# Kernel tuning notes

Measured on AMD Instinct MI355X. Metric: run time of the kernel, lower is better.

The kernel has to match this reference:

```python
import jax, jax.numpy as jnp
import numpy as np

PRIOR = 0.2
TEMP = 1.0
THRESHOLD = 0.5
B, L, D, H = 8, 4096, 768, 512


def setup_inputs() -> dict:
    key = jax.random.key(0)
    k1, k2, k3, k4 = jax.random.split(key, 4)
    hidden = jax.random.normal(k1, (B, L, D), jnp.float32)
    # MLP params: Linear(D,H) -> ReLU -> Linear(H,1)
    W1 = jax.random.normal(k2, (D, H), jnp.float32) / np.sqrt(D).astype(np.float32)
    b1 = jnp.zeros((H,), jnp.float32)
    W2 = jax.random.normal(k3, (H, 1), jnp.float32) / np.sqrt(H).astype(np.float32)
    b2 = jnp.zeros((1,), jnp.float32)
    # pre-sampled uniform noise for the RelaxedBernoulli logistic reparameterization
    noise_u = jax.random.uniform(k4, (B, L), jnp.float32, minval=1e-6, maxval=1.0 - 1e-6)
    return dict(hidden=hidden, W1=W1, b1=b1, W2=W2, b2=b2, noise_u=noise_u)


def reference(hidden, W1, b1, W2, b2, noise_u):
    bs, seq_len, model_dim = hidden.shape
    # boundary MLP -> per-token logits [B, L]
    h = jax.nn.relu(jnp.einsum('bld,dh->blh', hidden, W1) + b1)
    logits = (jnp.einsum('blh,ho->blo', h, W2) + b2)[..., 0]
    # RelaxedBernoulli rsample: sigmoid((logits + logistic_noise) / temp),
    # since logit(sigmoid(logits)) == logits
    logistic_noise = jnp.log(noise_u) - jnp.log1p(-noise_u)
    soft_boundaries = jax.nn.sigmoid((logits + logistic_noise) / TEMP)
    hard_bin = (soft_boundaries > THRESHOLD).astype(soft_boundaries.dtype)
    # straight-through estimator
    hard_boundaries = soft_boundaries + jax.lax.stop_gradient(hard_bin - soft_boundaries)
    # segment id of each token: number of boundaries strictly before it
    # (boundary token is the last element of its segment)
    seg = (jnp.cumsum(hard_bin, axis=1) - hard_bin).astype(jnp.int32)  # [B, L] in [0, L)
    ids = (seg + seq_len * jnp.arange(bs, dtype=jnp.int32)[:, None]).reshape(-1)
    flat = hidden.reshape(bs * seq_len, model_dim)
    seg_sum = jax.ops.segment_sum(flat, ids, num_segments=bs * seq_len)
    seg_cnt = jax.ops.segment_sum(jnp.ones((bs * seq_len,), hidden.dtype), ids,
                                  num_segments=bs * seq_len)
    # mean pooling per segment; unused segment slots stay zero (padded to L segments,
    # equivalent to the torch [S,B,D]->transpose output up to zero padding)
    pooled = (seg_sum / jnp.maximum(seg_cnt, 1.0)[:, None]).reshape(bs, seq_len, model_dim)
    # hinge loss on boundary rate: penalize |rate - (prior+0.05)| beyond margin 0.05
    ratio = jnp.mean(hard_boundaries)
    loss = jax.nn.relu(jnp.abs(ratio - (PRIOR + 0.05)) - 0.05)
    num_boundaries = jnp.sum(hard_bin)
    total_positions = jnp.asarray(bs * seq_len, jnp.float32)
    return pooled, loss, num_boundaries, total_positions
```

## Files before the change

### kernel.cpp

```cpp
#include <hip/hip_runtime.h>
#include <math.h>

typedef __attribute__((ext_vector_type(8))) short short8;
typedef __attribute__((ext_vector_type(4))) float float4v;
typedef unsigned int uint;

#define BATCH 8
#define SEQ   4096
#define DIM   768
#define HID   512
#define M_TOK (BATCH * SEQ)

static __device__ __forceinline__ short f2bf_rne(float x) {
    unsigned int u = __float_as_uint(x);
    unsigned int r = (u + 0x7FFFu + ((u >> 16) & 1u)) >> 16;
    return (short)r;
}
static __device__ __forceinline__ uint pack_bf2(float a, float b) {
    return __builtin_amdgcn_perm(__float_as_uint(b), __float_as_uint(a), 0x07060302u);
}
union FragU { uint u[4]; short8 s; };
static __device__ __forceinline__ void gl2lds16(const void* g, void* l) {
    __builtin_amdgcn_global_load_lds(
        (const __attribute__((address_space(1))) unsigned int*)g,
        (__attribute__((address_space(3))) unsigned int*)l, 16, 0, 0);
}

__global__ __launch_bounds__(256) void prep_kernel(const float* __restrict__ W1,
                                                   short* __restrict__ W1T) {
    __shared__ float t[64][65];
    const int bk = blockIdx.x % 12, bn = blockIdx.x / 12;
    const int k0 = bk * 64, n0 = bn * 64;
    const int tr = threadIdx.x >> 6, tc = threadIdx.x & 63;
#pragma unroll
    for (int i = 0; i < 16; i++) {
        int k = tr + i * 4;
        t[k][tc] = W1[(size_t)(k0 + k) * HID + n0 + tc];
    }
    __syncthreads();
#pragma unroll
    for (int i = 0; i < 16; i++) {
        int n = tr + i * 4;
        W1T[(size_t)(n0 + n) * DIM + k0 + tc] = f2bf_rne(t[tc][n]);
    }
}

__global__ __launch_bounds__(512, 2) void mlp_kernel(const float* __restrict__ A,
                                                     const short* __restrict__ BT,
                                                     const float* __restrict__ b1,
                                                     const float* __restrict__ W2,
                                                     float* __restrict__ logits) {
    extern __shared__ char smem[];
    const int tid = threadIdx.x, wave = tid >> 6, lane = tid & 63;
    const int q = lane >> 4, r = lane & 15;
    const int wr = wave >> 2, wc = wave & 3;
    const int m0 = blockIdx.x * 128;
    const int s7 = r & 7;

    char* rng0 = smem;
    char* rng1 = smem + 32768;
    char* Bb   = smem + 65536;

    const float* aSrc[4];
    int aD[4];
#pragma unroll
    for (int j = 0; j < 4; j++) {
        int i = wave * 4 + j;
        int row = i * 4 + (lane >> 4);
        int kc = (lane & 15) ^ (row & 7);
        aSrc[j] = A + (size_t)(m0 + row) * DIM + kc * 4;
        aD[j] = i * 1024;
    }
    const short* bSrc[8];
    int bD[8];
#pragma unroll
    for (int j = 0; j < 8; j++) {
        int i = wave * 8 + j;
        int n = i * 8 + (lane >> 3);
        int c = (lane & 7) ^ (n & 7);
        bSrc[j] = BT + (size_t)n * DIM + c * 8;
        bD[j] = i * 1024;
    }

    int aOff[2][2];
#pragma unroll
    for (int kk = 0; kk < 2; kk++)
#pragma unroll
        for (int c = 0; c < 2; c++)
            aOff[kk][c] = (wr * 64 + r) * 256 + (((kk * 8 + q * 2 + c) ^ s7) * 16);
    int bOff[2];
#pragma unroll
    for (int kk = 0; kk < 2; kk++)
        bOff[kk] = (wc * 128 + r) * 128 + (((kk * 4 + q) ^ s7) * 16);

    float4v acc[4][8] = {};

    auto stageA = [&](int t, char* rb) {
        const int ko = t * 64;
#pragma unroll
        for (int j = 0; j < 4; j++) gl2lds16(aSrc[j] + ko, rb + aD[j]);
    };
    auto stageB = [&](int t) {
        const int ko = t * 64;
#pragma unroll
        for (int j = 0; j < 8; j++) gl2lds16(bSrc[j] + ko, Bb + bD[j]);
    };
    auto compute = [&](const char* ab) {
#pragma unroll
        for (int kk = 0; kk < 2; kk++) {
            short8 bfr[8];
#pragma unroll
            for (int nf = 0; nf < 8; nf++)
                bfr[nf] = *(const short8*)(Bb + bOff[kk] + nf * 2048);
#pragma unroll
            for (int mf = 0; mf < 4; mf++) {
                float4v f0 = *(const float4v*)(ab + aOff[kk][0] + mf * 4096);
                float4v f1 = *(const float4v*)(ab + aOff[kk][1] + mf * 4096);
                FragU af;
                af.u[0] = pack_bf2(f0[0], f0[1]);
                af.u[1] = pack_bf2(f0[2], f0[3]);
                af.u[2] = pack_bf2(f1[0], f1[1]);
                af.u[3] = pack_bf2(f1[2], f1[3]);
#pragma unroll
                for (int nf = 0; nf < 8; nf++)
                    acc[mf][nf] = __builtin_amdgcn_mfma_f32_16x16x32_bf16(
                        af.s, bfr[nf], acc[mf][nf], 0, 0, 0);
            }
        }
    };

    stageB(0);
    stageA(0, rng0);
    stageA(1, rng1);

    for (int t = 0; t < 11; ++t) {
        asm volatile("s_waitcnt vmcnt(4)" ::: "memory");
        __builtin_amdgcn_s_barrier();
        __builtin_amdgcn_sched_barrier(0);
        compute((t & 1) ? rng1 : rng0);
        __builtin_amdgcn_sched_barrier(0);
        __builtin_amdgcn_s_barrier();
        stageB(t + 1);
        if (t <= 9) stageA(t + 2, (t & 1) ? rng1 : rng0);
    }
    asm volatile("s_waitcnt vmcnt(0)" ::: "memory");
    __builtin_amdgcn_s_barrier();
    __builtin_amdgcn_sched_barrier(0);
    compute(rng1);
    __syncthreads();

    float b1v[8], w2v[8];
#pragma unroll
    for (int nf = 0; nf < 8; nf++) {
        int gc = wc * 128 + nf * 16 + r;
        b1v[nf] = b1[gc];
        w2v[nf] = W2[gc];
    }
    float* red = (float*)smem;
#pragma unroll
    for (int mf = 0; mf < 4; mf++)
#pragma unroll
        for (int v = 0; v < 4; v++) {
            float pp = 0.f;
#pragma unroll
            for (int nf = 0; nf < 8; nf++) {
                float hh = acc[mf][nf][v] + b1v[nf];
                hh = hh > 0.f ? hh : 0.f;
                pp += hh * w2v[nf];
            }
#pragma unroll
            for (int off = 1; off < 16; off <<= 1) pp += __shfl_xor(pp, off, 64);
            if (r == 0) red[wc * 128 + wr * 64 + mf * 16 + q * 4 + v] = pp;
        }
    __syncthreads();
    if (tid < 128) {
        logits[m0 + tid] = red[tid] + red[128 + tid] + red[256 + tid] + red[384 + tid];
    }
}

__global__ __launch_bounds__(1024) void boundary_kernel(const float* __restrict__ logits,
                                                        const float* __restrict__ b2p,
                                                        const float* __restrict__ noise,
                                                        int* __restrict__ starts,
                                                        int* __restrict__ nseg,
                                                        int* __restrict__ nbcount) {
    const int b = blockIdx.x, tid = threadIdx.x;
    const int base = tid * 4;
    const float b2 = b2p[0];
    int h[4], c = 0;
#pragma unroll
    for (int j = 0; j < 4; j++) {
        int l = base + j;
        float u = noise[b * SEQ + l];
        float lg = logits[b * SEQ + l] + b2 + logf(u) - log1pf(-u);
        h[j] = (lg > 0.f) ? 1 : 0;
        c += h[j];
    }
    const int lane = tid & 63, wid = tid >> 6;
    int inc = c;
    for (int off = 1; off < 64; off <<= 1) {
        int t = __shfl_up(inc, off, 64);
        if (lane >= off) inc += t;
    }
    __shared__ int wtot[16], woff[16], extra[2];
    if (lane == 63) wtot[wid] = inc;
    if (tid == 1023) extra[0] = h[3];
    __syncthreads();
    if (tid == 0) {
        int s = 0;
        for (int i = 0; i < 16; i++) { woff[i] = s; s += wtot[i]; }
        extra[1] = s;
    }
    __syncthreads();
    int run = (inc - c) + woff[wid];
#pragma unroll
    for (int j = 0; j < 4; j++) {
        int l = base + j;
        if (h[j]) {
            run++;
            if (l < SEQ - 1) starts[b * (SEQ + 1) + run] = l + 1;
        }
    }
    if (tid == 0) {
        int total = extra[1];
        int ns = total + (extra[0] ? 0 : 1);
        starts[b * (SEQ + 1)] = 0;
        starts[b * (SEQ + 1) + ns] = SEQ;
        nseg[b] = ns;
        nbcount[b] = total;
    }
}

__global__ __launch_bounds__(256) void pool_kernel(const float* __restrict__ hidden,
                                                   const int* __restrict__ starts,
                                                   const int* __restrict__ nseg,
                                                   float* __restrict__ out) {
    const int wid = threadIdx.x >> 6, lane = threadIdx.x & 63;
    const int s = blockIdx.x * 4 + wid, b = blockIdx.y;
    float* orow = out + (size_t)(b * SEQ + s) * DIM;
    float4v a0 = {0.f, 0.f, 0.f, 0.f}, a1 = a0, a2 = a0;
    const int ns = nseg[b];
    if (s < ns) {
        const int st = starts[b * (SEQ + 1) + s];
        const int en = starts[b * (SEQ + 1) + s + 1];
        float4v c0 = a0, c1 = a0, c2 = a0;
        const float* hbase = hidden + (size_t)(b * SEQ) * DIM;
        int row = st;
        for (; row + 2 <= en; row += 2) {
            const float* h0 = hbase + (size_t)row * DIM;
            const float* h1 = h0 + DIM;
            a0 += *(const float4v*)(h0 + lane * 4);
            a1 += *(const float4v*)(h0 + (lane + 64) * 4);
            a2 += *(const float4v*)(h0 + (lane + 128) * 4);
            c0 += *(const float4v*)(h1 + lane * 4);
            c1 += *(const float4v*)(h1 + (lane + 64) * 4);
            c2 += *(const float4v*)(h1 + (lane + 128) * 4);
        }
        if (row < en) {
            const float* h0 = hbase + (size_t)row * DIM;
            a0 += *(const float4v*)(h0 + lane * 4);
            a1 += *(const float4v*)(h0 + (lane + 64) * 4);
            a2 += *(const float4v*)(h0 + (lane + 128) * 4);
        }
        a0 += c0; a1 += c1; a2 += c2;
        const float invc = 1.f / (float)(en - st);
        a0 *= invc; a1 *= invc; a2 *= invc;
    }
    __builtin_nontemporal_store(a0, (float4v*)(orow + lane * 4));
    __builtin_nontemporal_store(a1, (float4v*)(orow + (lane + 64) * 4));
    __builtin_nontemporal_store(a2, (float4v*)(orow + (lane + 128) * 4));
}

__global__ void finalize_kernel(const int* __restrict__ nbcount, float* __restrict__ tail) {
    int nb = 0;
    for (int i = 0; i < BATCH; i++) nb += nbcount[i];
    float ratio = (float)nb / (float)M_TOK;
    float d = fabsf(ratio - 0.25f) - 0.05f;
    tail[0] = d > 0.f ? d : 0.f;
    tail[1] = (float)nb;
    tail[2] = (float)M_TOK;
}

#define MLP_LDS 131072
extern "C" void kernel_launch(void* const* d_in, const int* in_sizes, int n_in,
                              void* d_out, int out_size, void* d_ws, size_t ws_size,
                              hipStream_t stream) {
    const float* hidden = (const float*)d_in[0];
    const float* W1     = (const float*)d_in[1];
    const float* b1     = (const float*)d_in[2];
    const float* W2     = (const float*)d_in[3];
    const float* b2     = (const float*)d_in[4];
    const float* noise  = (const float*)d_in[5];

    char* ws = (char*)d_ws;
    short* W1T    = (short*)(ws);
    float* logits = (float*)(ws + 786432);
    int*   starts = (int*)(ws + 917504);
    int*   nseg   = (int*)(ws + 917504 + 131104);
    int*   nbcount = nseg + 8;
    float* out    = (float*)d_out;

    static bool s_mlp_attr = false;
    if (!s_mlp_attr) {
        hipFuncSetAttribute(reinterpret_cast<const void*>(mlp_kernel),
                            hipFuncAttributeMaxDynamicSharedMemorySize, MLP_LDS);
        s_mlp_attr = true;
    }

    prep_kernel<<<96, 256, 0, stream>>>(W1, W1T);
    mlp_kernel<<<M_TOK / 128, 512, MLP_LDS, stream>>>(hidden, W1T, b1, W2, logits);
    boundary_kernel<<<BATCH, 1024, 0, stream>>>(logits, b2, noise, starts, nseg, nbcount);
    pool_kernel<<<dim3(SEQ / 4, BATCH), 256, 0, stream>>>(hidden, starts, nseg, out);
    finalize_kernel<<<1, 1, 0, stream>>>(nbcount, out + (size_t)M_TOK * DIM);
}
```

Before: 225.3 us.

## Pre-swizzle W1 into MFMA fragment order and load B directly to registers

The prep kernel now writes bf16 W1 in an order where each 64-lane wave can load one MFMA B fragment with a single contiguous dwordx4 per lane. The MLP kernel drops the LDS staging of B and loads B fragments straight from global memory (mostly L2) into registers each k-step. This halves LDS use, which may allow more blocks per CU. The cost is more global traffic per wave and exposed load latency inside each iteration.

Result: slower. 262.9 us (+16.7%).

```diff
diff --git a/kernel.cpp b/kernel.cpp
--- a/kernel.cpp
+++ b/kernel.cpp
@@ -3,6 +3,7 @@
 
 typedef __attribute__((ext_vector_type(8))) short short8;
 typedef __attribute__((ext_vector_type(4))) float float4v;
+typedef __attribute__((ext_vector_type(4))) int   int4v;
 typedef unsigned int uint;
 
 #define BATCH 8
@@ -19,30 +20,29 @@
 static __device__ __forceinline__ uint pack_bf2(float a, float b) {
     return __builtin_amdgcn_perm(__float_as_uint(b), __float_as_uint(a), 0x07060302u);
 }
-union FragU { uint u[4]; short8 s; };
+union FragU { uint u[4]; short8 s; int4v i4; };
 static __device__ __forceinline__ void gl2lds16(const void* g, void* l) {
     __builtin_amdgcn_global_load_lds(
         (const __attribute__((address_space(1))) unsigned int*)g,
         (__attribute__((address_space(3))) unsigned int*)l, 16, 0, 0);
 }
 
-__global__ __launch_bounds__(256) void prep_kernel(const float* __restrict__ W1,
-                                                   short* __restrict__ W1T) {
-    __shared__ float t[64][65];
-    const int bk = blockIdx.x % 12, bn = blockIdx.x / 12;
-    const int k0 = bk * 64, n0 = bn * 64;
-    const int tr = threadIdx.x >> 6, tc = threadIdx.x & 63;
-#pragma unroll
-    for (int i = 0; i < 16; i++) {
-        int k = tr + i * 4;
-        t[k][tc] = W1[(size_t)(k0 + k) * HID + n0 + tc];
-    }
-    __syncthreads();
-#pragma unroll
-    for (int i = 0; i < 16; i++) {
-        int n = tr + i * 4;
-        W1T[(size_t)(n0 + n) * DIM + k0 + tc] = f2bf_rne(t[tc][n]);
-    }
+__global__ __launch_bounds__(64) void prep_kernel(const float* __restrict__ W1,
+                                                  short* __restrict__ W1T) {
+    const int bid = blockIdx.x;
+    const int h = bid / 24, kg = bid % 24;
+    const int lane = threadIdx.x & 63, q = lane >> 4, r = lane & 15;
+    float f[8];
+#pragma unroll
+    for (int j = 0; j < 8; j++)
+        f[j] = W1[(size_t)(kg * 32 + q * 8 + j) * HID + h * 16 + r];
+    uint u[4];
+#pragma unroll
+    for (int i = 0; i < 4; i++)
+        u[i] = ((uint)(unsigned short)f2bf_rne(f[2 * i + 1]) << 16) |
+               (uint)(unsigned short)f2bf_rne(f[2 * i]);
+    uint* dst = (uint*)(W1T + (size_t)bid * 512) + lane * 4;
+    dst[0] = u[0]; dst[1] = u[1]; dst[2] = u[2]; dst[3] = u[3];
 }
 
 __global__ __launch_bounds__(512, 2) void mlp_kernel(const float* __restrict__ A,
@@ -59,7 +59,6 @@
 
     char* rng0 = smem;
     char* rng1 = smem + 32768;
-    char* Bb   = smem + 65536;
 
     const float* aSrc[4];
     int aD[4];
@@ -71,27 +70,12 @@
         aSrc[j] = A + (size_t)(m0 + row) * DIM + kc * 4;
         aD[j] = i * 1024;
     }
-    const short* bSrc[8];
-    int bD[8];
-#pragma unroll
-    for (int j = 0; j < 8; j++) {
-        int i = wave * 8 + j;
-        int n = i * 8 + (lane >> 3);
-        int c = (lane & 7) ^ (n & 7);
-        bSrc[j] = BT + (size_t)n * DIM + c * 8;
-        bD[j] = i * 1024;
-    }
-
     int aOff[2][2];
 #pragma unroll
     for (int kk = 0; kk < 2; kk++)
 #pragma unroll
         for (int c = 0; c < 2; c++)
             aOff[kk][c] = (wr * 64 + r) * 256 + (((kk * 8 + q * 2 + c) ^ s7) * 16);
-    int bOff[2];
-#pragma unroll
-    for (int kk = 0; kk < 2; kk++)
-        bOff[kk] = (wc * 128 + r) * 128 + (((kk * 4 + q) ^ s7) * 16);
 
     float4v acc[4][8] = {};
 
@@ -100,54 +84,61 @@
 #pragma unroll
         for (int j = 0; j < 4; j++) gl2lds16(aSrc[j] + ko, rb + aD[j]);
     };
-    auto stageB = [&](int t) {
-        const int ko = t * 64;
-#pragma unroll
-        for (int j = 0; j < 8; j++) gl2lds16(bSrc[j] + ko, Bb + bD[j]);
-    };
-    auto compute = [&](const char* ab) {
-#pragma unroll
-        for (int kk = 0; kk < 2; kk++) {
-            short8 bfr[8];
-#pragma unroll
-            for (int nf = 0; nf < 8; nf++)
-                bfr[nf] = *(const short8*)(Bb + bOff[kk] + nf * 2048);
+
+    auto iter = [&](const char* ab, int t, char* sb, bool doStage) {
+        asm volatile("s_waitcnt vmcnt(4)" ::: "memory");
+        __builtin_amdgcn_s_barrier();
+        __builtin_amdgcn_sched_barrier(0);
+        FragU bFu[2][8];
+#pragma unroll
+        for (int kk = 0; kk < 2; kk++)
+#pragma unroll
+            for (int nf = 0; nf < 8; nf++) {
+                const short* p = BT + (((size_t)((wc * 8 + nf) * 24 + t * 2 + kk)) << 9)
+                               + lane * 8;
+                asm volatile("global_load_dwordx4 %0, %1, off"
+                             : "=v"(bFu[kk][nf].i4) : "v"(p) : "memory");
+            }
+        FragU aFu[2][4];
+#pragma unroll
+        for (int kk = 0; kk < 2; kk++)
 #pragma unroll
             for (int mf = 0; mf < 4; mf++) {
                 float4v f0 = *(const float4v*)(ab + aOff[kk][0] + mf * 4096);
                 float4v f1 = *(const float4v*)(ab + aOff[kk][1] + mf * 4096);
-                FragU af;
-                af.u[0] = pack_bf2(f0[0], f0[1]);
-                af.u[1] = pack_bf2(f0[2], f0[3]);
-                af.u[2] = pack_bf2(f1[0], f1[1]);
-                af.u[3] = pack_bf2(f1[2], f1[3]);
-#pragma unroll
-                for (int nf = 0; nf < 8; nf++)
-                    acc[mf][nf] = __builtin_amdgcn_mfma_f32_16x16x32_bf16(
-                        af.s, bfr[nf], acc[mf][nf], 0, 0, 0);
+                aFu[kk][mf].u[0] = pack_bf2(f0[0], f0[1]);
+                aFu[kk][mf].u[1] = pack_bf2(f0[2], f0[3]);
+                aFu[kk][mf].u[2] = pack_bf2(f1[0], f1[1]);
+                aFu[kk][mf].u[3] = pack_bf2(f1[2], f1[3]);
             }
-        }
+        asm volatile("s_waitcnt vmcnt(8)" ::: "memory");
+        __builtin_amdgcn_sched_barrier(0);
+#pragma unroll
+        for (int mf = 0; mf < 4; mf++)
+#pragma unroll
+            for (int nf = 0; nf < 8; nf++)
+                acc[mf][nf] = __builtin_amdgcn_mfma_f32_16x16x32_bf16(
+                    aFu[0][mf].s, bFu[0][nf].s, acc[mf][nf], 0, 0, 0);
+        asm volatile("s_waitcnt vmcnt(0)" ::: "memory");
+        __builtin_amdgcn_sched_barrier(0);
+#pragma unroll
+        for (int mf = 0; mf < 4; mf++)
+#pragma unroll
+            for (int nf = 0; nf < 8; nf++)
+                acc[mf][nf] = __builtin_amdgcn_mfma_f32_16x16x32_bf16(
+                    aFu[1][mf].s, bFu[1][nf].s, acc[mf][nf], 0, 0, 0);
+        __builtin_amdgcn_s_barrier();
+        if (doStage) stageA(t + 2, sb);
     };
 
-    stageB(0);
     stageA(0, rng0);
     stageA(1, rng1);
-
-    for (int t = 0; t < 11; ++t) {
-        asm volatile("s_waitcnt vmcnt(4)" ::: "memory");
-        __builtin_amdgcn_s_barrier();
-        __builtin_amdgcn_sched_barrier(0);
-        compute((t & 1) ? rng1 : rng0);
-        __builtin_amdgcn_sched_barrier(0);
-        __builtin_amdgcn_s_barrier();
-        stageB(t + 1);
-        if (t <= 9) stageA(t + 2, (t & 1) ? rng1 : rng0);
-    }
-    asm volatile("s_waitcnt vmcnt(0)" ::: "memory");
-    __builtin_amdgcn_s_barrier();
-    __builtin_amdgcn_sched_barrier(0);
-    compute(rng1);
-    __syncthreads();
+    for (int tb = 0; tb < 10; tb += 2) {
+        iter(rng0, tb, rng0, true);
+        iter(rng1, tb + 1, rng1, true);
+    }
+    iter(rng0, 10, rng0, false);
+    iter(rng1, 11, rng1, false);
 
     float b1v[8], w2v[8];
 #pragma unroll
@@ -156,6 +147,7 @@
         b1v[nf] = b1[gc];
         w2v[nf] = W2[gc];
     }
+    __syncthreads();
     float* red = (float*)smem;
 #pragma unroll
     for (int mf = 0; mf < 4; mf++)
@@ -281,7 +273,7 @@
     tail[2] = (float)M_TOK;
 }
 
-#define MLP_LDS 131072
+#define MLP_LDS 65536
 extern "C" void kernel_launch(void* const* d_in, const int* in_sizes, int n_in,
                               void* d_out, int out_size, void* d_ws, size_t ws_size,
                               hipStream_t stream) {
@@ -307,7 +299,7 @@
         s_mlp_attr = true;
     }
 
-    prep_kernel<<<96, 256, 0, stream>>>(W1, W1T);
+    prep_kernel<<<768, 64, 0, stream>>>(W1, W1T);
     mlp_kernel<<<M_TOK / 128, 512, MLP_LDS, stream>>>(hidden, W1T, b1, W2, logits);
     boundary_kernel<<<BATCH, 1024, 0, stream>>>(logits, b2, noise, starts, nseg, nbcount);
     pool_kernel<<<dim3(SEQ / 4, BATCH), 256, 0, stream>>>(hidden, starts, nseg, out);
```
